# Performance work log

Hardware: AMD Instinct MI355X
Metric: run time of the kernel (lower is better)

## Reference

```python
import jax, jax.numpy as jnp
import numpy as np

D_MODEL = 1024
NUM_HEADS = 16
HEAD_DIM = D_MODEL // NUM_HEADS


def setup_inputs() -> dict:
    key = jax.random.key(0)
    ks = jax.random.split(key, 5)
    x = jax.random.normal(ks[0], (2, 2048, D_MODEL), dtype=jnp.float32)
    s = 1.0 / np.sqrt(D_MODEL)
    # nn.Linear weight is [out, in]; y = x @ W.T
    Wq = jax.random.normal(ks[1], (D_MODEL, D_MODEL), dtype=jnp.float32) * s
    Wk = jax.random.normal(ks[2], (D_MODEL, D_MODEL), dtype=jnp.float32) * s
    Wv = jax.random.normal(ks[3], (D_MODEL, D_MODEL), dtype=jnp.float32) * s
    Wo = jax.random.normal(ks[4], (D_MODEL, D_MODEL), dtype=jnp.float32) * s
    return {"x": x, "Wq": Wq, "Wk": Wk, "Wv": Wv, "Wo": Wo}


def reference(x, Wq, Wk, Wv, Wo):
    b, s, d = x.shape
    h, hd = NUM_HEADS, HEAD_DIM
    # projections (Linear: x @ W.T), reshape to [b, h, s, hd]
    def proj(W):
        return (x @ W.T).reshape(b, s, h, hd).transpose(0, 2, 1, 3)
    Q, K, V = proj(Wq), proj(Wk), proj(Wv)
    # NOTE: original scales by 1/sqrt(d_model), not 1/sqrt(head_dim)
    scores = jnp.einsum('bhqd,bhkd->bhqk', Q, K) / jnp.sqrt(jnp.float32(d))
    attn = jax.nn.softmax(scores, axis=-1)
    ctx = jnp.einsum('bhqk,bhkd->bhqd', attn, V)
    ctx = ctx.transpose(0, 2, 1, 3).reshape(b, s, d)
    return ctx @ Wo.T
```

## Files before the change

kernel.cpp:

```cpp
#include <hip/hip_runtime.h>
#include <cstddef>
#include <cstdint>

#define SEQ 2048
#define DM 1024
#define NH 16
#define HD 64

typedef _Float16 f16;
typedef __attribute__((ext_vector_type(8))) _Float16 f16x8;
typedef __attribute__((ext_vector_type(4))) _Float16 f16x4;
typedef __attribute__((ext_vector_type(2))) _Float16 f16x2;
typedef __attribute__((ext_vector_type(2))) __fp16 hf16x2;
typedef __attribute__((ext_vector_type(4))) float f32x4;

__global__ __launch_bounds__(256) void cast_kernel(const float* __restrict__ in,
                                                   f16* __restrict__ out, int n4) {
  int i = blockIdx.x * 256 + threadIdx.x;
  if (i < n4) {
    float4 v = ((const float4*)in)[i];
    f16x4 o = {(f16)v.x, (f16)v.y, (f16)v.z, (f16)v.w};
    ((f16x4*)out)[i] = o;
  }
}

__device__ __forceinline__ void gload16(const void* g, void* lds) {
  __builtin_amdgcn_global_load_lds((const __attribute__((address_space(1))) void*)g,
                                   (__attribute__((address_space(3))) void*)lds,
                                   16, 0, 0);
}

__device__ __forceinline__ void gemm_tile(const f16* __restrict__ A,
                                          const f16* __restrict__ B,
                                          f16* As, f16* Bs,
                                          int K, f32x4 acc[4][4]) {
  const int t = threadIdx.x;
  const int lane = t & 63;
  const int w = t >> 6;
  const int wm = (w & 1) << 6, wn = (w >> 1) << 6;
  const int srow = lane >> 2, scol = lane & 3;
  const int fr = lane & 15, q = lane >> 4;
  for (int k0 = 0; k0 < K; k0 += 32) {
    __syncthreads();
#pragma unroll
    for (int c = 0; c < 2; ++c) {
      const int chunk = (w << 1) + c;
      const int row = (chunk << 4) + srow;
      gload16(A + (size_t)row * K + k0 + (scol << 3), As + (chunk << 9));
      gload16(B + (size_t)row * K + k0 + (scol << 3), Bs + (chunk << 9));
    }
    __syncthreads();
    f16x8 af[4], bfr[4];
#pragma unroll
    for (int i = 0; i < 4; ++i)
      af[i] = *(const f16x8*)(As + (wm + (i << 4) + fr) * 32 + (q << 3));
#pragma unroll
    for (int j = 0; j < 4; ++j)
      bfr[j] = *(const f16x8*)(Bs + (wn + (j << 4) + fr) * 32 + (q << 3));
#pragma unroll
    for (int i = 0; i < 4; ++i)
#pragma unroll
      for (int j = 0; j < 4; ++j)
        acc[i][j] = __builtin_amdgcn_mfma_f32_16x16x32_f16(af[i], bfr[j],
                                                           acc[i][j], 0, 0, 0);
  }
}

#define QSCALE 0.04508422003f
__global__ __launch_bounds__(256) void gemm_qkv(
    const f16* __restrict__ xb, const f16* __restrict__ Wqb,
    const f16* __restrict__ Wkb, const f16* __restrict__ Wvb,
    f16* __restrict__ Qb, f16* __restrict__ Kb, f16* __restrict__ Vtg) {
  __shared__ f16 As[128 * 32];
  __shared__ f16 Bs[128 * 32];
  const int which = blockIdx.x >> 3;
  const int bn = (blockIdx.x & 7) << 7;
  const int bm = blockIdx.y << 7;
  const f16* B = (which == 0) ? Wqb : (which == 1) ? Wkb : Wvb;
  f32x4 acc[4][4] = {};
  gemm_tile(xb + (size_t)bm * DM, B + (size_t)bn * DM, As, Bs, DM, acc);
  const int lane = threadIdx.x & 63, w = threadIdx.x >> 6;
  const int wm = (w & 1) << 6, wn = (w >> 1) << 6;
  const int col = lane & 15, q = lane >> 4;
  if (which < 2) {
    f16* C = (which == 0) ? Qb : Kb;
    const float sc = (which == 0) ? QSCALE : 1.0f;
#pragma unroll
    for (int i = 0; i < 4; ++i) {
      const int m = bm + wm + (i << 4) + (q << 2);
#pragma unroll
      for (int j = 0; j < 4; ++j) {
        const int n = bn + wn + (j << 4) + col;
#pragma unroll
        for (int r = 0; r < 4; ++r)
          C[(size_t)(m + r) * DM + n] = (f16)(acc[i][j][r] * sc);
      }
    }
  } else {
#pragma unroll
    for (int i = 0; i < 4; ++i) {
      const int m = bm + wm + (i << 4) + (q << 2);
      const int b = m >> 11, s = m & 2047;
#pragma unroll
      for (int j = 0; j < 4; ++j) {
        const int n = bn + wn + (j << 4) + col;
        const int h = n >> 6, d = n & 63;
        f16x4 o = {(f16)acc[i][j][0], (f16)acc[i][j][1],
                   (f16)acc[i][j][2], (f16)acc[i][j][3]};
        *(f16x4*)(Vtg + (((size_t)(b * NH + h) * HD + d) * SEQ + s)) = o;
      }
    }
  }
}

__global__ __launch_bounds__(256) void gemm_out(const f16* __restrict__ Ab,
                                                const f16* __restrict__ Wob,
                                                float* __restrict__ out) {
  __shared__ f16 As[128 * 32];
  __shared__ f16 Bs[128 * 32];
  const int bn = blockIdx.x << 7, bm = blockIdx.y << 7;
  f32x4 acc[4][4] = {};
  gemm_tile(Ab + (size_t)bm * DM, Wob + (size_t)bn * DM, As, Bs, DM, acc);
  const int lane = threadIdx.x & 63, w = threadIdx.x >> 6;
  const int wm = (w & 1) << 6, wn = (w >> 1) << 6;
  const int col = lane & 15, q = lane >> 4;
#pragma unroll
  for (int i = 0; i < 4; ++i) {
    const int m = bm + wm + (i << 4) + (q << 2);
#pragma unroll
    for (int j = 0; j < 4; ++j) {
      const int n = bn + wn + (j << 4) + col;
#pragma unroll
      for (int r = 0; r < 4; ++r)
        out[(size_t)(m + r) * DM + n] = acc[i][j][r];
    }
  }
}

__global__ __launch_bounds__(256) void attn_mfma(const f16* __restrict__ Qb,
                                                 const f16* __restrict__ Kb,
                                                 const f16* __restrict__ Vtg,
                                                 f16* __restrict__ Ctx) {
  __shared__ f16 smem[8192];
  f16* Ks = smem;
  f16* Vs = smem + 4096;
  const int t = threadIdx.x, lane = t & 63, w = t >> 6;
  const int fr = lane & 15, quad = lane >> 4;
  const int qt16 = blockIdx.x & 15;
  const int h = (blockIdx.x >> 4) & 15, b = blockIdx.x >> 8;

  const size_t qrow0 = (size_t)b * SEQ + qt16 * 128 + w * 32;

  f16x8 Qf[2][2];
#pragma unroll
  for (int qt = 0; qt < 2; ++qt)
#pragma unroll
    for (int hf = 0; hf < 2; ++hf)
      Qf[qt][hf] = *(const f16x8*)(Qb + (qrow0 + qt * 16 + fr) * DM + h * HD +
                                   hf * 32 + (quad << 3));

  const f16* Kg = Kb + ((size_t)b * SEQ + 16 * w + (lane >> 2)) * DM + h * HD +
                  (lane & 3) * 8;
  const f16* Vg = Vtg + (((size_t)(b * NH + h) * HD) + 16 * w + (lane >> 2)) * SEQ +
                  (((lane & 3) ^ ((lane >> 2) & 3)) << 3);
  f16* KsD0 = Ks + w * 512;
  f16* KsD1 = Ks + 2048 + w * 512;
  f16* VsD0 = Vs + w * 512;
  f16* VsD1 = Vs + 2048 + w * 512;

  f32x4 acc[2][4] = {};
  float lacc[2] = {0.f, 0.f};

  for (int kt = 0; kt < 32; ++kt) {
    const size_t ko = (size_t)kt * 64;
    __syncthreads();
    gload16(Kg + ko * DM, KsD0);
    gload16(Kg + ko * DM + 32, KsD1);
    gload16(Vg + ko, VsD0);
    gload16(Vg + ko + 32, VsD1);
    __syncthreads();

    f16x8 Kf[4][2];
#pragma unroll
    for (int mt = 0; mt < 4; ++mt)
#pragma unroll
      for (int hf = 0; hf < 2; ++hf)
        Kf[mt][hf] = *(const f16x8*)(Ks + hf * 2048 + (mt * 16 + fr) * 32 +
                                     (quad << 3));

    f16x4 pf[2][4];
#pragma unroll
    for (int qt = 0; qt < 2; ++qt) {
      f32x4 z[4] = {};
#pragma unroll
      for (int mt = 0; mt < 4; ++mt) {
        z[mt] = __builtin_amdgcn_mfma_f32_16x16x32_f16(Kf[mt][0], Qf[qt][0],
                                                       z[mt], 0, 0, 0);
        z[mt] = __builtin_amdgcn_mfma_f32_16x16x32_f16(Kf[mt][1], Qf[qt][1],
                                                       z[mt], 0, 0, 0);
      }
#pragma unroll
      for (int mt = 0; mt < 4; ++mt) {
        const float p0 = __builtin_amdgcn_exp2f(z[mt][0]);
        const float p1 = __builtin_amdgcn_exp2f(z[mt][1]);
        const float p2 = __builtin_amdgcn_exp2f(z[mt][2]);
        const float p3 = __builtin_amdgcn_exp2f(z[mt][3]);
        lacc[qt] += (p0 + p1) + (p2 + p3);
        const f16x2 lo = __builtin_bit_cast(f16x2, __builtin_amdgcn_cvt_pkrtz(p0, p1));
        const f16x2 hi = __builtin_bit_cast(f16x2, __builtin_amdgcn_cvt_pkrtz(p2, p3));
        f16x4 pv; pv.x = lo.x; pv.y = lo.y; pv.z = hi.x; pv.w = hi.y;
        pf[qt][mt] = pv;
      }
    }

#pragma unroll
    for (int dt = 0; dt < 4; ++dt) {
#pragma unroll
      for (int kc = 0; kc < 4; ++kc) {
        const int gg = (((kc & 1) << 1) + (quad >> 1)) ^ (fr & 3);
        const f16x4 vf = *(const f16x4*)(Vs + ((kc >> 1) * 4 + dt) * 512 +
                                         fr * 32 + (gg << 3) + ((quad & 1) << 2));
#pragma unroll
        for (int qt = 0; qt < 2; ++qt)
          acc[qt][dt] = __builtin_amdgcn_mfma_f32_16x16x16f16(vf, pf[qt][kc],
                                                              acc[qt][dt], 0, 0, 0);
      }
    }
  }

  float inv[2];
#pragma unroll
  for (int qt = 0; qt < 2; ++qt) {
    float l = lacc[qt];
    l += __shfl_xor(l, 16);
    l += __shfl_xor(l, 32);
    inv[qt] = __builtin_amdgcn_rcpf(l);
  }

  __syncthreads();
  f16* T = smem + w * 2048;
#pragma unroll
  for (int qt = 0; qt < 2; ++qt)
#pragma unroll
    for (int dt = 0; dt < 4; ++dt)
#pragma unroll
      for (int r = 0; r < 4; ++r)
        T[(qt * 16 + fr) * 64 + dt * 16 + (quad << 2) + r] =
            (f16)(acc[qt][dt][r] * inv[qt]);
#pragma unroll
  for (int p = 0; p < 4; ++p) {
    const int ql = p * 8 + (lane >> 3);
    const f16x8 v = *(const f16x8*)(T + ql * 64 + ((lane & 7) << 3));
    *(f16x8*)(Ctx + (qrow0 + ql) * DM + h * HD + ((lane & 7) << 3)) = v;
  }
}

extern "C" void kernel_launch(void* const* d_in, const int* in_sizes, int n_in,
                              void* d_out, int out_size, void* d_ws, size_t ws_size,
                              hipStream_t stream) {
  const float* x  = (const float*)d_in[0];
  const float* Wq = (const float*)d_in[1];
  const float* Wk = (const float*)d_in[2];
  const float* Wv = (const float*)d_in[3];
  const float* Wo = (const float*)d_in[4];

  char* ws = (char*)d_ws;
  f16* xb  = (f16*)(ws);
  f16* Wqb = (f16*)(ws + (8u << 20));
  f16* Wkb = (f16*)(ws + (10u << 20));
  f16* Wvb = (f16*)(ws + (12u << 20));
  f16* Wob = (f16*)(ws + (14u << 20));
  f16* Qb  = (f16*)(ws + (16u << 20));
  f16* Kb  = (f16*)(ws + (24u << 20));
  f16* Vtg = (f16*)(ws + (32u << 20));
  f16* Ctx = (f16*)(ws + (40u << 20));

  cast_kernel<<<4096, 256, 0, stream>>>(x, xb, 1048576);
  cast_kernel<<<1024, 256, 0, stream>>>(Wq, Wqb, 262144);
  cast_kernel<<<1024, 256, 0, stream>>>(Wk, Wkb, 262144);
  cast_kernel<<<1024, 256, 0, stream>>>(Wv, Wvb, 262144);
  cast_kernel<<<1024, 256, 0, stream>>>(Wo, Wob, 262144);

  gemm_qkv<<<dim3(24, 32), 256, 0, stream>>>(xb, Wqb, Wkb, Wvb, Qb, Kb, Vtg);
  attn_mfma<<<dim3(2 * NH * (SEQ / 128)), 256, 0, stream>>>(Qb, Kb, Vtg, Ctx);
  gemm_out<<<dim3(8, 32), 256, 0, stream>>>(Ctx, Wob, (float*)d_out);
}
```

Before: 203.2 us.

## Double-buffer attention K/V, coalesce V-transpose stores, merge weight casts, remap blocks

Attention now keeps two K/V shared-memory buffers and prefetches the next key tile while the current one is computed, with one barrier per iteration instead of two. The V projection epilogue transposes through shared memory so each thread writes a 16-byte contiguous chunk of V^T rather than scattered 8-byte stores. The four weight-cast launches become one 2D launch into a contiguous buffer. The attention block index is also remapped to spread batch-head pairs across consecutive blocks. The price is doubled LDS per attention block, which may reduce occupancy, and the prefetch relies on the async LDS loads having completed at the next barrier.

```diff
diff --git a/kernel.cpp b/kernel.cpp
--- a/kernel.cpp
+++ b/kernel.cpp
@@ -11,7 +11,6 @@
 typedef __attribute__((ext_vector_type(8))) _Float16 f16x8;
 typedef __attribute__((ext_vector_type(4))) _Float16 f16x4;
 typedef __attribute__((ext_vector_type(2))) _Float16 f16x2;
-typedef __attribute__((ext_vector_type(2))) __fp16 hf16x2;
 typedef __attribute__((ext_vector_type(4))) float f32x4;
 
 __global__ __launch_bounds__(256) void cast_kernel(const float* __restrict__ in,
@@ -22,6 +21,19 @@
     f16x4 o = {(f16)v.x, (f16)v.y, (f16)v.z, (f16)v.w};
     ((f16x4*)out)[i] = o;
   }
+}
+
+__global__ __launch_bounds__(256) void cast_w4(const float* __restrict__ Wq,
+                                               const float* __restrict__ Wk,
+                                               const float* __restrict__ Wv,
+                                               const float* __restrict__ Wo,
+                                               f16* __restrict__ out) {
+  const int i = blockIdx.x * 256 + threadIdx.x;
+  const int y = blockIdx.y;
+  const float* src = (y == 0) ? Wq : (y == 1) ? Wk : (y == 2) ? Wv : Wo;
+  float4 v = ((const float4*)src)[i];
+  f16x4 o = {(f16)v.x, (f16)v.y, (f16)v.z, (f16)v.w};
+  ((f16x4*)(out + (size_t)y * 1048576))[i] = o;
 }
 
 __device__ __forceinline__ void gload16(const void* g, void* lds) {
@@ -71,8 +83,9 @@
     const f16* __restrict__ xb, const f16* __restrict__ Wqb,
     const f16* __restrict__ Wkb, const f16* __restrict__ Wvb,
     f16* __restrict__ Qb, f16* __restrict__ Kb, f16* __restrict__ Vtg) {
-  __shared__ f16 As[128 * 32];
-  __shared__ f16 Bs[128 * 32];
+  __shared__ f16 smem[16384];
+  f16* As = smem;
+  f16* Bs = smem + 4096;
   const int which = blockIdx.x >> 3;
   const int bn = (blockIdx.x & 7) << 7;
   const int bm = blockIdx.y << 7;
@@ -97,18 +110,27 @@
       }
     }
   } else {
+    __syncthreads();
 #pragma unroll
     for (int i = 0; i < 4; ++i) {
-      const int m = bm + wm + (i << 4) + (q << 2);
-      const int b = m >> 11, s = m & 2047;
+      const int cm = ((wm + (i << 4)) >> 3) + (q >> 1);
 #pragma unroll
       for (int j = 0; j < 4; ++j) {
-        const int n = bn + wn + (j << 4) + col;
-        const int h = n >> 6, d = n & 63;
+        const int nl = wn + (j << 4) + col;
         f16x4 o = {(f16)acc[i][j][0], (f16)acc[i][j][1],
                    (f16)acc[i][j][2], (f16)acc[i][j][3]};
-        *(f16x4*)(Vtg + (((size_t)(b * NH + h) * HD + d) * SEQ + s)) = o;
-      }
+        *(f16x4*)(smem + nl * 128 + ((cm ^ (nl & 15)) << 3) + ((q & 1) << 2)) = o;
+      }
+    }
+    __syncthreads();
+    const int b = bm >> 11, sbase = bm & 2047;
+#pragma unroll
+    for (int p = 0; p < 8; ++p) {
+      const int nl = p * 16 + w * 4 + (lane >> 4);
+      const int cmc = lane & 15;
+      const f16x8 v = *(const f16x8*)(smem + nl * 128 + ((cmc ^ (nl & 15)) << 3));
+      const int h = (bn + nl) >> 6, d = (bn + nl) & 63;
+      *(f16x8*)(Vtg + ((size_t)(b * NH + h) * HD + d) * SEQ + sbase + cmc * 8) = v;
     }
   }
 }
@@ -141,13 +163,14 @@
                                                  const f16* __restrict__ Kb,
                                                  const f16* __restrict__ Vtg,
                                                  f16* __restrict__ Ctx) {
-  __shared__ f16 smem[8192];
-  f16* Ks = smem;
-  f16* Vs = smem + 4096;
+  __shared__ f16 smem[16384];
   const int t = threadIdx.x, lane = t & 63, w = t >> 6;
   const int fr = lane & 15, quad = lane >> 4;
-  const int qt16 = blockIdx.x & 15;
-  const int h = (blockIdx.x >> 4) & 15, b = blockIdx.x >> 8;
+  const int i = blockIdx.x;
+  const int j = i >> 3;
+  const int bh = ((i & 7) << 2) + (j >> 4);
+  const int qt16 = j & 15;
+  const int b = bh >> 4, h = bh & 15;
 
   const size_t qrow0 = (size_t)b * SEQ + qt16 * 128 + w * 32;
 
@@ -163,22 +186,27 @@
                   (lane & 3) * 8;
   const f16* Vg = Vtg + (((size_t)(b * NH + h) * HD) + 16 * w + (lane >> 2)) * SEQ +
                   (((lane & 3) ^ ((lane >> 2) & 3)) << 3);
-  f16* KsD0 = Ks + w * 512;
-  f16* KsD1 = Ks + 2048 + w * 512;
-  f16* VsD0 = Vs + w * 512;
-  f16* VsD1 = Vs + 2048 + w * 512;
 
   f32x4 acc[2][4] = {};
   float lacc[2] = {0.f, 0.f};
 
+  auto stage = [&](int kt, int buf) {
+    const size_t ko = (size_t)kt * 64;
+    f16* Kd = smem + buf * 4096 + w * 512;
+    f16* Vd = smem + 8192 + buf * 4096 + w * 512;
+    gload16(Kg + ko * DM, Kd);
+    gload16(Kg + ko * DM + 32, Kd + 2048);
+    gload16(Vg + ko, Vd);
+    gload16(Vg + ko + 32, Vd + 2048);
+  };
+
+  stage(0, 0);
   for (int kt = 0; kt < 32; ++kt) {
-    const size_t ko = (size_t)kt * 64;
-    __syncthreads();
-    gload16(Kg + ko * DM, KsD0);
-    gload16(Kg + ko * DM + 32, KsD1);
-    gload16(Vg + ko, VsD0);
-    gload16(Vg + ko + 32, VsD1);
-    __syncthreads();
+    const int cur = kt & 1;
+    __syncthreads();
+    if (kt < 31) stage(kt + 1, cur ^ 1);
+    const f16* Ks = smem + cur * 4096;
+    const f16* Vs = smem + 8192 + cur * 4096;
 
     f16x8 Kf[4][2];
 #pragma unroll
@@ -266,20 +294,18 @@
 
   char* ws = (char*)d_ws;
   f16* xb  = (f16*)(ws);
-  f16* Wqb = (f16*)(ws + (8u << 20));
-  f16* Wkb = (f16*)(ws + (10u << 20));
-  f16* Wvb = (f16*)(ws + (12u << 20));
-  f16* Wob = (f16*)(ws + (14u << 20));
+  f16* Wb  = (f16*)(ws + (8u << 20));
+  f16* Wqb = Wb;
+  f16* Wkb = Wb + 1048576;
+  f16* Wvb = Wb + 2097152;
+  f16* Wob = Wb + 3145728;
   f16* Qb  = (f16*)(ws + (16u << 20));
   f16* Kb  = (f16*)(ws + (24u << 20));
   f16* Vtg = (f16*)(ws + (32u << 20));
   f16* Ctx = (f16*)(ws + (40u << 20));
 
   cast_kernel<<<4096, 256, 0, stream>>>(x, xb, 1048576);
-  cast_kernel<<<1024, 256, 0, stream>>>(Wq, Wqb, 262144);
-  cast_kernel<<<1024, 256, 0, stream>>>(Wk, Wkb, 262144);
-  cast_kernel<<<1024, 256, 0, stream>>>(Wv, Wvb, 262144);
-  cast_kernel<<<1024, 256, 0, stream>>>(Wo, Wob, 262144);
+  cast_w4<<<dim3(1024, 4), 256, 0, stream>>>(Wq, Wk, Wv, Wo, Wb);
 
   gemm_qkv<<<dim3(24, 32), 256, 0, stream>>>(xb, Wqb, Wkb, Wvb, Qb, Kb, Vtg);
   attn_mfma<<<dim3(2 * NH * (SEQ / 128)), 256, 0, stream>>>(Qb, Kb, Vtg, Ctx);
```

Result: no change. 204.6 us (+0.7%).
